# Performance work log

Measured on AMD Instinct MI355X. Metric: run time of the kernel, lower is better.

The kernel has to match this reference:

```python
import jax, jax.numpy as jnp
from jax import lax
import numpy as np

D = 8        # domain_num
L = 12       # label_num
C = 9        # attr_num
W = 128      # window_size
B = 4096
EPS = 1e-5


def setup_inputs() -> dict:
    key = jax.random.key(0)
    ks = jax.random.split(key, 12)
    s = 0.05
    return {
        "x": jax.random.normal(ks[0], (B, C, 1, W), dtype=jnp.float32),
        "weights": jax.random.uniform(ks[1], (B, D), dtype=jnp.float32),
        # per-domain stacked parameters (leading dim D)
        "gamma": jnp.ones((D, C), dtype=jnp.float32),
        "beta": jnp.zeros((D, C), dtype=jnp.float32),
        "w1": jax.random.normal(ks[2], (D, 32, C, 9), dtype=jnp.float32) * s,
        "b1": jax.random.normal(ks[3], (D, 32), dtype=jnp.float32) * s,
        "w2": jax.random.normal(ks[4], (D, 64, 32, 9), dtype=jnp.float32) * s,
        "b2": jax.random.normal(ks[5], (D, 64), dtype=jnp.float32) * s,
        "fcw": jax.random.normal(ks[6], (D, L, 64 * 26), dtype=jnp.float32) * s,
        "fcb": jax.random.normal(ks[7], (D, L), dtype=jnp.float32) * s,
    }


def _maxpool2(h):
    # MaxPool along width, kernel 2 stride 2 (height is 1 and already squeezed)
    b, c, w = h.shape
    return h.reshape(b, c, w // 2, 2).max(axis=-1)


def _branch(x3, gamma, beta, w1, b1, w2, b2, fcw, fcb):
    # x3: [B, C, W]. BatchNorm2d in training mode: batch stats over (N, H, W).
    mean = x3.mean(axis=(0, 2), keepdims=True)
    var = x3.var(axis=(0, 2), keepdims=True)
    xn = (x3 - mean) * lax.rsqrt(var + EPS) * gamma[None, :, None] + beta[None, :, None]
    dn = ('NCH', 'OIH', 'NCH')
    h = lax.conv_general_dilated(xn, w1, (1,), 'VALID', dimension_numbers=dn)
    h = _maxpool2(jax.nn.relu(h + b1[None, :, None]))          # [B,32,60]
    h = lax.conv_general_dilated(h, w2, (1,), 'VALID', dimension_numbers=dn)
    h = _maxpool2(jax.nn.relu(h + b2[None, :, None]))          # [B,64,26]
    flat = h.reshape(h.shape[0], 64 * 26)
    return jax.nn.relu(flat @ fcw.T + fcb)                      # [B,L]


def reference(x, weights, gamma, beta, w1, b1, w2, b2, fcw, fcb):
    x3 = x[:, :, 0, :]  # squeeze height=1 -> [B,C,W]
    per_domain = jax.vmap(_branch, in_axes=(None, 0, 0, 0, 0, 0, 0, 0, 0))(
        x3, gamma, beta, w1, b1, w2, b2, fcw, fcb)              # [D,B,L]
    # vectorized form of the nested python-loop weighted sum over domains
    return jnp.einsum('bd,dbl->bl', weights, per_domain)        # [B,L]
```

## Files before the change

### kernel.cpp

```cpp
#include <hip/hip_runtime.h>
#include <hip/hip_bf16.h>

#define D 8
#define L 12
#define C 9
#define W 128
#define B 4096
#define EPS 1e-5f

typedef __attribute__((ext_vector_type(8))) short v8s;
typedef __attribute__((ext_vector_type(4))) float v4f;

#define OFF_STATS 0
#define OFF_B1E   18432
#define OFF_W1T   18688
#define OFF_W2T   39168
#define OFF_FCWP  112896
#define OFF_XG    192768
#define WS_XG_FLOATS (OFF_XG + (B * 2304) / 2)

#define REGION 2336

__device__ inline unsigned short f2bf(float f) {
    unsigned u = __builtin_bit_cast(unsigned, f);
    u += 0x7FFFu + ((u >> 16) & 1u);
    return (unsigned short)(u >> 16);
}
__device__ inline unsigned pk2(float a, float b) {
    float2 f2; f2.x = a; f2.y = b;
    __hip_bfloat162 h = __float22bfloat162_rn(f2);
    unsigned u; __builtin_memcpy(&u, &h, 4);
    return u;
}
__device__ inline void gl_lds16(const void* g, void* l) {
    __builtin_amdgcn_global_load_lds(
        (const __attribute__((address_space(1))) void*)g,
        (__attribute__((address_space(3))) void*)l, 16, 0, 0);
}
__device__ inline void gl_lds4(const void* g, void* l) {
    __builtin_amdgcn_global_load_lds(
        (const __attribute__((address_space(1))) void*)g,
        (__attribute__((address_space(3))) void*)l, 4, 0, 0);
}

__global__ void stats_repack_kernel(const float* __restrict__ x,
                                    const float* __restrict__ w2,
                                    const float* __restrict__ fcw,
                                    float* __restrict__ ws,
                                    float* __restrict__ out,
                                    int use_xg) {
    const int t = threadIdx.x;
    __shared__ float red2[4][18];
    if (blockIdx.x < 1024) {
        const int rb = blockIdx.x * 4;
        const int w = t & 127, half = t >> 7;
        float s[9], s2[9];
        #pragma unroll
        for (int c = 0; c < 9; c++) { s[c] = 0.f; s2[c] = 0.f; }
        #pragma unroll
        for (int pass = 0; pass < 2; pass++) {
            const int row = rb + pass * 2 + half;
            const float* xr = x + (size_t)row * 1152 + w;
            float v[9];
            #pragma unroll
            for (int c = 0; c < 9; c++) {
                v[c] = xr[c * 128];
                s[c] += v[c]; s2[c] += v[c] * v[c];
            }
            if (use_xg) {
                short* xgr = (short*)(ws + OFF_XG) + (size_t)row * 2304;
                uint4 lo, hi;
                lo.x = pk2(v[0], v[1]); lo.y = pk2(v[2], v[3]);
                lo.z = pk2(v[4], v[5]); lo.w = pk2(v[6], v[7]);
                hi.x = (unsigned)(unsigned short)f2bf(v[8]); hi.y = 0; hi.z = 0; hi.w = 0;
                *(uint4*)&xgr[w * 8] = lo;
                *(uint4*)&xgr[(144 + w) * 8] = hi;
            }
        }
        if (use_xg && t < 128) {
            const int row = rb + (t >> 5), j = t & 31;
            uint4 z; z.x = z.y = z.z = z.w = 0;
            *(uint4*)&((short*)(ws + OFF_XG))[(size_t)row * 2304 +
                                              ((j >> 4) * 144 + 128 + (j & 15)) * 8] = z;
        }
        #pragma unroll
        for (int c = 0; c < 9; c++) {
            #pragma unroll
            for (int off = 32; off >= 1; off >>= 1) {
                s[c]  += __shfl_down(s[c], off);
                s2[c] += __shfl_down(s2[c], off);
            }
        }
        if ((t & 63) == 0) {
            #pragma unroll
            for (int c = 0; c < 9; c++) {
                red2[t >> 6][c] = s[c]; red2[t >> 6][9 + c] = s2[c];
            }
        }
        __syncthreads();
        if (t < 18)
            ws[OFF_STATS + t * 1024 + blockIdx.x] =
                red2[0][t] + red2[1][t] + red2[2][t] + red2[3][t];
    } else if (blockIdx.x < 1152) {
        const int g = (blockIdx.x - 1024) * 4 + (t >> 6);
        const int lane = t & 63;
        const int d = g >> 6, o = g & 63;
        const float* src = w2 + (size_t)(d * 64 + o) * 288;
        short* dst = (short*)(ws + OFF_W2T) + (size_t)d * 18432 + o * 288;
        for (int i = lane; i < 288; i += 64) {
            int ic = i / 9, tap = i % 9;
            dst[tap * 32 + ic] = (short)f2bf(src[i]);
        }
    } else if (blockIdx.x < 1200) {
        const int g = (blockIdx.x - 1152) * 4 + (t >> 6);
        const int lane = t & 63;
        const int dl = g >> 1, half = g & 1;
        const float* src = fcw + (size_t)dl * 1664;
        short* dst = (short*)(ws + OFF_FCWP) + (size_t)dl * 1664;
        for (int i = half * 832 + lane; i < half * 832 + 832; i += 64) {
            int o = i / 26, p = i % 26;
            dst[p * 64 + o] = (short)f2bf(src[i]);
        }
    } else {
        const int base = (blockIdx.x - 1200) * 6144;
        float4 z; z.x = z.y = z.z = z.w = 0.f;
        float4* o4 = (float4*)(out + base);
        for (int i = t; i < 1536; i += 256) o4[i] = z;
    }
}

__global__ void fold1_kernel(const float* __restrict__ w1, const float* __restrict__ b1,
                             const float* __restrict__ gamma, const float* __restrict__ beta,
                             float* __restrict__ ws) {
    const int d = blockIdx.x, t = threadIdx.x;
    __shared__ float redA[8];
    __shared__ float g[9], bt[9];
    for (int c = 0; c < 9; c++) {
        float s = 0.f, s2 = 0.f;
        #pragma unroll
        for (int j = 0; j < 4; j++) {
            s  += ws[OFF_STATS + c * 1024 + t + 256 * j];
            s2 += ws[OFF_STATS + (9 + c) * 1024 + t + 256 * j];
        }
        #pragma unroll
        for (int off = 32; off >= 1; off >>= 1) {
            s  += __shfl_down(s, off);
            s2 += __shfl_down(s2, off);
        }
        if ((t & 63) == 0) { redA[(t >> 6) * 2] = s; redA[(t >> 6) * 2 + 1] = s2; }
        __syncthreads();
        if (t == 0) {
            float st  = redA[0] + redA[2] + redA[4] + redA[6];
            float st2 = redA[1] + redA[3] + redA[5] + redA[7];
            const float N = (float)B * (float)W;
            float m  = st / N;
            float vv = st2 / N - m * m;
            float inv = rsqrtf(vv + EPS);
            float gg = gamma[d * 9 + c] * inv;
            g[c] = gg; bt[c] = beta[d * 9 + c] - gg * m;
        }
        __syncthreads();
    }
    const int o = t >> 3, sub = t & 7;
    short* w1t = (short*)(ws + OFF_W1T);
    short* dst = w1t + (size_t)d * 5120 + o * 160;
    const float* src = w1 + ((size_t)(d * 32 + o)) * 81;
    float bias_part = 0.f;
    for (int tap = sub; tap < 10; tap += 8) {
        for (int c = 0; c < 16; c++) {
            float v = 0.f;
            if (tap < 9 && c < 9) {
                float wv = src[c * 9 + tap];
                v = wv * g[c];
                bias_part += wv * bt[c];
            }
            dst[tap * 16 + c] = (short)f2bf(v);
        }
    }
    bias_part += __shfl_xor(bias_part, 1);
    bias_part += __shfl_xor(bias_part, 2);
    bias_part += __shfl_xor(bias_part, 4);
    if (sub == 0) ws[OFF_B1E + d * 32 + o] = b1[d * 32 + o] + bias_part;
}

template<bool XG>
__global__ __launch_bounds__(256, 4)
void branch_kernel(const float* __restrict__ x,
                   const float* __restrict__ b2g,
                   const float* __restrict__ fcb,
                   const float* __restrict__ wts,
                   const float* __restrict__ ws,
                   float* __restrict__ out) {
    const int t = threadIdx.x;
    const int lane = t & 63;
    const int wv = t >> 6;
    const int d = blockIdx.y;
    const int b0 = blockIdx.x * 4;
    const short* w1t  = (const short*)(ws + OFF_W1T) + (size_t)d * 5120;
    const short* w2t  = (const short*)(ws + OFF_W2T) + (size_t)d * 18432;
    const short* fcwp = (const short*)(ws + OFF_FCWP) + (size_t)d * 12 * 1664;
    const float* b1e  = ws + OFF_B1E + d * 32;

    __shared__ __align__(16) short lds[4 * REGION];
    short* myr = &lds[wv * REGION];

    const int n = lane & 15, quad = lane >> 4;

    if (XG) {
        const char* xgrow = (const char*)(ws + OFF_XG) + (size_t)(b0 + wv) * 4608;
        char* lb = (char*)myr;
        #pragma unroll
        for (int k = 0; k < 4; k++)
            gl_lds16(xgrow + k * 1024 + lane * 16, lb + k * 1024);
        gl_lds4(xgrow + 4096 + lane * 4, lb + 4096);
        gl_lds4(xgrow + 4352 + lane * 4, lb + 4352);
        asm volatile("s_waitcnt vmcnt(0)" ::: "memory");
    } else {
        const float* xrow = x + (size_t)(b0 + wv) * 1152;
        #pragma unroll
        for (int rep = 0; rep < 2; rep++) {
            const int w = lane + rep * 64;
            float v[9];
            #pragma unroll
            for (int c = 0; c < 9; c++) v[c] = xrow[c * 128 + w];
            uint4 lo, hi;
            lo.x = pk2(v[0], v[1]); lo.y = pk2(v[2], v[3]);
            lo.z = pk2(v[4], v[5]); lo.w = pk2(v[6], v[7]);
            hi.x = (unsigned)(unsigned short)f2bf(v[8]); hi.y = 0; hi.z = 0; hi.w = 0;
            *(uint4*)&myr[(0 * 144 + w) * 8] = lo;
            *(uint4*)&myr[(1 * 144 + w) * 8] = hi;
        }
        if (lane < 16) {
            uint4 z; z.x = z.y = z.z = z.w = 0;
            *(uint4*)&myr[(0 * 144 + 128 + lane) * 8] = z;
            *(uint4*)&myr[(1 * 144 + 128 + lane) * 8] = z;
        }
    }

    {
        const int qh = quad >> 1, ql = quad & 1;
        const float bias0 = b1e[n], bias1 = b1e[16 + n];
        v4f acc[8][2];
        #pragma unroll
        for (int mt = 0; mt < 8; mt++)
            #pragma unroll
            for (int nt = 0; nt < 2; nt++) { v4f z = {0.f,0.f,0.f,0.f}; acc[mt][nt] = z; }
        #pragma unroll
        for (int s = 0; s < 5; s++) {
            v8s Bw0 = *(const v8s*)&w1t[n * 160 + (2 * s + qh) * 16 + ql * 8];
            v8s Bw1 = *(const v8s*)&w1t[(16 + n) * 160 + (2 * s + qh) * 16 + ql * 8];
            #pragma unroll
            for (int mt = 0; mt < 8; mt++) {
                const int row = mt * 16 + n + 2 * s + qh;
                v8s Af = *(const v8s*)&myr[(ql * 144 + row) * 8];
                acc[mt][0] = __builtin_amdgcn_mfma_f32_16x16x32_bf16(Af, Bw0, acc[mt][0], 0, 0, 0);
                acc[mt][1] = __builtin_amdgcn_mfma_f32_16x16x32_bf16(Af, Bw1, acc[mt][1], 0, 0, 0);
            }
        }
        unsigned held[16];
        #pragma unroll
        for (int mt = 0; mt < 8; mt++)
            #pragma unroll
            for (int nt = 0; nt < 2; nt++) {
                const float bb = nt ? bias1 : bias0;
                float h0  = fmaxf(fmaxf(acc[mt][nt][0], acc[mt][nt][1]) + bb, 0.f);
                float h1v = fmaxf(fmaxf(acc[mt][nt][2], acc[mt][nt][3]) + bb, 0.f);
                held[mt * 2 + nt] = pk2(h0, h1v);
            }
        #pragma unroll
        for (int mt = 0; mt < 8; mt++) {
            const int p = mt * 8 + quad * 2;
            #pragma unroll
            for (int nt = 0; nt < 2; nt++) {
                const unsigned pr = held[mt * 2 + nt];
                const int plane = nt * 2 + (n >> 3);
                const int col = n & 7;
                if (p < 60)     myr[(plane * 73 + p) * 8 + col]     = (short)(pr & 0xFFFFu);
                if (p + 1 < 60) myr[(plane * 73 + p + 1) * 8 + col] = (short)(pr >> 16);
            }
        }
    }

    {
        float biasv[4];
        #pragma unroll
        for (int nt = 0; nt < 4; nt++) biasv[nt] = b2g[d * 64 + nt * 16 + n];
        v4f acc[4][4];
        #pragma unroll
        for (int mt = 0; mt < 4; mt++)
            #pragma unroll
            for (int nt = 0; nt < 4; nt++) { v4f z = {0.f,0.f,0.f,0.f}; acc[mt][nt] = z; }
        for (int tap = 0; tap < 9; tap++) {
            v8s Bw[4];
            #pragma unroll
            for (int nt = 0; nt < 4; nt++)
                Bw[nt] = *(const v8s*)&w2t[(nt * 16 + n) * 288 + tap * 32 + quad * 8];
            #pragma unroll
            for (int mt = 0; mt < 4; mt++) {
                const int row = mt * 16 + n + tap;
                v8s Af = *(const v8s*)&myr[(quad * 73 + row) * 8];
                #pragma unroll
                for (int nt = 0; nt < 4; nt++)
                    acc[mt][nt] = __builtin_amdgcn_mfma_f32_16x16x32_bf16(Af, Bw[nt], acc[mt][nt], 0, 0, 0);
            }
        }
        unsigned held[16];
        #pragma unroll
        for (int mt = 0; mt < 4; mt++)
            #pragma unroll
            for (int nt = 0; nt < 4; nt++) {
                float h0  = fmaxf(fmaxf(acc[mt][nt][0], acc[mt][nt][1]) + biasv[nt], 0.f);
                float h1v = fmaxf(fmaxf(acc[mt][nt][2], acc[mt][nt][3]) + biasv[nt], 0.f);
                held[mt * 4 + nt] = pk2(h0, h1v);
            }
        #pragma unroll
        for (int mt = 0; mt < 4; mt++) {
            const int p = mt * 8 + quad * 2;
            #pragma unroll
            for (int nt = 0; nt < 4; nt++) {
                const unsigned pr = held[mt * 4 + nt];
                const int oc = nt * 16 + n;
                if (p < 26) {
                    const int gs = (oc >> 3) ^ (p & 7);
                    myr[p * 64 + gs * 8 + (oc & 7)] = (short)(pr & 0xFFFFu);
                }
                if (p + 1 < 26) {
                    const int gs = (oc >> 3) ^ ((p + 1) & 7);
                    myr[(p + 1) * 64 + gs * 8 + (oc & 7)] = (short)(pr >> 16);
                }
            }
        }
    }
    __syncthreads();

    {
        const int lrow = (n < 12) ? n : 0;
        v4f acc = {0.f, 0.f, 0.f, 0.f};
        for (int ks = wv; ks < 52; ks += 4) {
            const int p = ks >> 1;
            const int gs = ((ks & 1) * 4 + quad) ^ (p & 7);
            v8s A  = *(const v8s*)&fcwp[lrow * 1664 + ks * 32 + quad * 8];
            v8s Bf = *(const v8s*)&lds[(n & 3) * REGION + p * 64 + gs * 8];
            acc = __builtin_amdgcn_mfma_f32_16x16x32_bf16(A, Bf, acc, 0, 0, 0);
        }
        float* red = (float*)(myr + 1672);
        *(float4*)&red[lane * 4] = *(float4*)&acc;
    }
    __syncthreads();
    if (t < 64) {
        float sum[4] = {0.f, 0.f, 0.f, 0.f};
        #pragma unroll
        for (int w = 0; w < 4; w++) {
            const float* redw = (const float*)(&lds[w * REGION + 1672]);
            float4 v = *(const float4*)&redw[lane * 4];
            sum[0] += v.x; sum[1] += v.y; sum[2] += v.z; sum[3] += v.w;
        }
        if (n < 4) {
            const float wgt = wts[(size_t)(b0 + n) * 8 + d];
            #pragma unroll
            for (int r = 0; r < 4; r++) {
                const int l = quad * 4 + r;
                if (l < 12) {
                    float v = fmaxf(sum[r] + fcb[d * 12 + l], 0.f);
                    atomicAdd(&out[(size_t)(b0 + n) * 12 + l], wgt * v);
                }
            }
        }
    }
}

extern "C" void kernel_launch(void* const* d_in, const int* in_sizes, int n_in,
                              void* d_out, int out_size, void* d_ws, size_t ws_size,
                              hipStream_t stream) {
    const float* x       = (const float*)d_in[0];
    const float* weights = (const float*)d_in[1];
    const float* gamma   = (const float*)d_in[2];
    const float* beta    = (const float*)d_in[3];
    const float* w1      = (const float*)d_in[4];
    const float* b1      = (const float*)d_in[5];
    const float* w2      = (const float*)d_in[6];
    const float* b2      = (const float*)d_in[7];
    const float* fcw     = (const float*)d_in[8];
    const float* fcb     = (const float*)d_in[9];
    float* ws  = (float*)d_ws;
    float* out = (float*)d_out;

    const int use_xg = (ws_size >= (size_t)WS_XG_FLOATS * 4) ? 1 : 0;

    stats_repack_kernel<<<dim3(1208), 256, 0, stream>>>(x, w2, fcw, ws, out, use_xg);
    fold1_kernel<<<dim3(D), 256, 0, stream>>>(w1, b1, gamma, beta, ws);
    if (use_xg)
        branch_kernel<true><<<dim3(B / 4, D), 256, 0, stream>>>(x, b2, fcb, weights, ws, out);
    else
        branch_kernel<false><<<dim3(B / 4, D), 256, 0, stream>>>(x, b2, fcb, weights, ws, out);
}
```

Baseline: 248.7 us.

## Drop bf16 x pre-pack path, raise wave priority around MFMA loops, simplify fold reduction

Removes the pre-packed bf16 copy of x in workspace, so the stats kernel no longer writes it and the branch kernel always loads fp32 x directly and converts it in-kernel. Adds s_setprio around the MFMA loops so waves issuing matrix work get scheduling priority. Changes fold1 so each wave reduces whole channels, removing the per-channel block barriers. The trade is less global write traffic up front against more per-block x reads and conversion (x is re-read by all 8 domain blocks).

```diff
diff --git a/kernel.cpp b/kernel.cpp
--- a/kernel.cpp
+++ b/kernel.cpp
@@ -16,8 +16,6 @@
 #define OFF_W1T   18688
 #define OFF_W2T   39168
 #define OFF_FCWP  112896
-#define OFF_XG    192768
-#define WS_XG_FLOATS (OFF_XG + (B * 2304) / 2)
 
 #define REGION 2336
 
@@ -32,23 +30,12 @@
     unsigned u; __builtin_memcpy(&u, &h, 4);
     return u;
 }
-__device__ inline void gl_lds16(const void* g, void* l) {
-    __builtin_amdgcn_global_load_lds(
-        (const __attribute__((address_space(1))) void*)g,
-        (__attribute__((address_space(3))) void*)l, 16, 0, 0);
-}
-__device__ inline void gl_lds4(const void* g, void* l) {
-    __builtin_amdgcn_global_load_lds(
-        (const __attribute__((address_space(1))) void*)g,
-        (__attribute__((address_space(3))) void*)l, 4, 0, 0);
-}
 
 __global__ void stats_repack_kernel(const float* __restrict__ x,
                                     const float* __restrict__ w2,
                                     const float* __restrict__ fcw,
                                     float* __restrict__ ws,
-                                    float* __restrict__ out,
-                                    int use_xg) {
+                                    float* __restrict__ out) {
     const int t = threadIdx.x;
     __shared__ float red2[4][18];
     if (blockIdx.x < 1024) {
@@ -61,27 +48,11 @@
         for (int pass = 0; pass < 2; pass++) {
             const int row = rb + pass * 2 + half;
             const float* xr = x + (size_t)row * 1152 + w;
-            float v[9];
             #pragma unroll
             for (int c = 0; c < 9; c++) {
-                v[c] = xr[c * 128];
-                s[c] += v[c]; s2[c] += v[c] * v[c];
-            }
-            if (use_xg) {
-                short* xgr = (short*)(ws + OFF_XG) + (size_t)row * 2304;
-                uint4 lo, hi;
-                lo.x = pk2(v[0], v[1]); lo.y = pk2(v[2], v[3]);
-                lo.z = pk2(v[4], v[5]); lo.w = pk2(v[6], v[7]);
-                hi.x = (unsigned)(unsigned short)f2bf(v[8]); hi.y = 0; hi.z = 0; hi.w = 0;
-                *(uint4*)&xgr[w * 8] = lo;
-                *(uint4*)&xgr[(144 + w) * 8] = hi;
-            }
-        }
-        if (use_xg && t < 128) {
-            const int row = rb + (t >> 5), j = t & 31;
-            uint4 z; z.x = z.y = z.z = z.w = 0;
-            *(uint4*)&((short*)(ws + OFF_XG))[(size_t)row * 2304 +
-                                              ((j >> 4) * 144 + 128 + (j & 15)) * 8] = z;
+                float v = xr[c * 128];
+                s[c] += v; s2[c] += v * v;
+            }
         }
         #pragma unroll
         for (int c = 0; c < 9; c++) {
@@ -133,34 +104,30 @@
                              const float* __restrict__ gamma, const float* __restrict__ beta,
                              float* __restrict__ ws) {
     const int d = blockIdx.x, t = threadIdx.x;
-    __shared__ float redA[8];
+    const int lane = t & 63, wv = t >> 6;
     __shared__ float g[9], bt[9];
-    for (int c = 0; c < 9; c++) {
+    for (int c = wv; c < 9; c += 4) {
         float s = 0.f, s2 = 0.f;
         #pragma unroll
-        for (int j = 0; j < 4; j++) {
-            s  += ws[OFF_STATS + c * 1024 + t + 256 * j];
-            s2 += ws[OFF_STATS + (9 + c) * 1024 + t + 256 * j];
+        for (int j = 0; j < 16; j++) {
+            s  += ws[OFF_STATS + c * 1024 + lane + 64 * j];
+            s2 += ws[OFF_STATS + (9 + c) * 1024 + lane + 64 * j];
         }
         #pragma unroll
         for (int off = 32; off >= 1; off >>= 1) {
             s  += __shfl_down(s, off);
             s2 += __shfl_down(s2, off);
         }
-        if ((t & 63) == 0) { redA[(t >> 6) * 2] = s; redA[(t >> 6) * 2 + 1] = s2; }
-        __syncthreads();
-        if (t == 0) {
-            float st  = redA[0] + redA[2] + redA[4] + redA[6];
-            float st2 = redA[1] + redA[3] + redA[5] + redA[7];
+        if (lane == 0) {
             const float N = (float)B * (float)W;
-            float m  = st / N;
-            float vv = st2 / N - m * m;
+            float m  = s / N;
+            float vv = s2 / N - m * m;
             float inv = rsqrtf(vv + EPS);
             float gg = gamma[d * 9 + c] * inv;
             g[c] = gg; bt[c] = beta[d * 9 + c] - gg * m;
         }
-        __syncthreads();
-    }
+    }
+    __syncthreads();
     const int o = t >> 3, sub = t & 7;
     short* w1t = (short*)(ws + OFF_W1T);
     short* dst = w1t + (size_t)d * 5120 + o * 160;
@@ -170,9 +137,9 @@
         for (int c = 0; c < 16; c++) {
             float v = 0.f;
             if (tap < 9 && c < 9) {
-                float wv = src[c * 9 + tap];
-                v = wv * g[c];
-                bias_part += wv * bt[c];
+                float wv2 = src[c * 9 + tap];
+                v = wv2 * g[c];
+                bias_part += wv2 * bt[c];
             }
             dst[tap * 16 + c] = (short)f2bf(v);
         }
@@ -183,7 +150,6 @@
     if (sub == 0) ws[OFF_B1E + d * 32 + o] = b1[d * 32 + o] + bias_part;
 }
 
-template<bool XG>
 __global__ __launch_bounds__(256, 4)
 void branch_kernel(const float* __restrict__ x,
                    const float* __restrict__ b2g,
@@ -206,16 +172,7 @@
 
     const int n = lane & 15, quad = lane >> 4;
 
-    if (XG) {
-        const char* xgrow = (const char*)(ws + OFF_XG) + (size_t)(b0 + wv) * 4608;
-        char* lb = (char*)myr;
-        #pragma unroll
-        for (int k = 0; k < 4; k++)
-            gl_lds16(xgrow + k * 1024 + lane * 16, lb + k * 1024);
-        gl_lds4(xgrow + 4096 + lane * 4, lb + 4096);
-        gl_lds4(xgrow + 4352 + lane * 4, lb + 4352);
-        asm volatile("s_waitcnt vmcnt(0)" ::: "memory");
-    } else {
+    {
         const float* xrow = x + (size_t)(b0 + wv) * 1152;
         #pragma unroll
         for (int rep = 0; rep < 2; rep++) {
@@ -245,6 +202,7 @@
         for (int mt = 0; mt < 8; mt++)
             #pragma unroll
             for (int nt = 0; nt < 2; nt++) { v4f z = {0.f,0.f,0.f,0.f}; acc[mt][nt] = z; }
+        __builtin_amdgcn_s_setprio(1);
         #pragma unroll
         for (int s = 0; s < 5; s++) {
             v8s Bw0 = *(const v8s*)&w1t[n * 160 + (2 * s + qh) * 16 + ql * 8];
@@ -257,6 +215,7 @@
                 acc[mt][1] = __builtin_amdgcn_mfma_f32_16x16x32_bf16(Af, Bw1, acc[mt][1], 0, 0, 0);
             }
         }
+        __builtin_amdgcn_s_setprio(0);
         unsigned held[16];
         #pragma unroll
         for (int mt = 0; mt < 8; mt++)
@@ -290,6 +249,7 @@
         for (int mt = 0; mt < 4; mt++)
             #pragma unroll
             for (int nt = 0; nt < 4; nt++) { v4f z = {0.f,0.f,0.f,0.f}; acc[mt][nt] = z; }
+        __builtin_amdgcn_s_setprio(1);
         for (int tap = 0; tap < 9; tap++) {
             v8s Bw[4];
             #pragma unroll
@@ -304,6 +264,7 @@
                     acc[mt][nt] = __builtin_amdgcn_mfma_f32_16x16x32_bf16(Af, Bw[nt], acc[mt][nt], 0, 0, 0);
             }
         }
+        __builtin_amdgcn_s_setprio(0);
         unsigned held[16];
         #pragma unroll
         for (int mt = 0; mt < 4; mt++)
@@ -336,6 +297,7 @@
     {
         const int lrow = (n < 12) ? n : 0;
         v4f acc = {0.f, 0.f, 0.f, 0.f};
+        __builtin_amdgcn_s_setprio(1);
         for (int ks = wv; ks < 52; ks += 4) {
             const int p = ks >> 1;
             const int gs = ((ks & 1) * 4 + quad) ^ (p & 7);
@@ -343,6 +305,7 @@
             v8s Bf = *(const v8s*)&lds[(n & 3) * REGION + p * 64 + gs * 8];
             acc = __builtin_amdgcn_mfma_f32_16x16x32_bf16(A, Bf, acc, 0, 0, 0);
         }
+        __builtin_amdgcn_s_setprio(0);
         float* red = (float*)(myr + 1672);
         *(float4*)&red[lane * 4] = *(float4*)&acc;
     }
@@ -385,12 +348,7 @@
     float* ws  = (float*)d_ws;
     float* out = (float*)d_out;
 
-    const int use_xg = (ws_size >= (size_t)WS_XG_FLOATS * 4) ? 1 : 0;
-
-    stats_repack_kernel<<<dim3(1208), 256, 0, stream>>>(x, w2, fcw, ws, out, use_xg);
+    stats_repack_kernel<<<dim3(1208), 256, 0, stream>>>(x, w2, fcw, ws, out);
     fold1_kernel<<<dim3(D), 256, 0, stream>>>(w1, b1, gamma, beta, ws);
-    if (use_xg)
-        branch_kernel<true><<<dim3(B / 4, D), 256, 0, stream>>>(x, b2, fcb, weights, ws, out);
-    else
-        branch_kernel<false><<<dim3(B / 4, D), 256, 0, stream>>>(x, b2, fcb, weights, ws, out);
-}
+    branch_kernel<<<dim3(B / 4, D), 256, 0, stream>>>(x, b2, fcb, weights, ws, out);
+}
```

New measurement: 236.6 us. 4.9% less time.
